# Kernel optimization log

Hardware: AMD Instinct MI355X
Metric: run time of the kernel (lower is better)

## Reference

```python
import jax, jax.numpy as jnp
import numpy as np

EPS = 1e-6
SIGMA = 0.5          # observation_noise_std
E, B, M, C = 64, 512, 128, 128  # episode, batch, memory_size, code_size


def setup_inputs() -> dict:
    key = jax.random.key(0)
    k1, k2 = jax.random.split(key)
    return {
        "input_encoded": jax.random.normal(k1, (E, B, C), dtype=jnp.float32),
        "memory_mean": jax.random.normal(k2, (M, C), dtype=jnp.float32),
        "memory_logvar": jnp.zeros((1,), dtype=jnp.float32),
    }


def reference(input_encoded, memory_mean, memory_logvar):
    # GPM.write_to_memory with direct_writing=False (sequential Kalman write).
    bsz = input_encoded.shape[1]
    prior_var = jnp.exp(memory_logvar) * jnp.ones((M,), input_encoded.dtype) + EPS  # (M,)
    prior_mean = jnp.broadcast_to(memory_mean, (bsz, M, C))                # (B,M,C)
    prior_cov = jnp.broadcast_to(jnp.diag(prior_var), (bsz, M, M))         # (B,M,M)
    eye_m = jnp.eye(M, dtype=input_encoded.dtype)

    def step(carry, z_i):            # z_i: (B,C)
        mean, cov = carry            # (B,M,C), (B,M,M)
        # _solve_w_mean (pseudoinverse=False): w = inv(M M^T + s^2 I) M z
        gram = jnp.einsum('bmc,bnc->bmn', mean, mean) + (SIGMA ** 2) * eye_m
        mz = jnp.einsum('bmc,bc->bm', mean, z_i)
        w = jnp.linalg.solve(gram, mz[..., None])[..., 0]  # (B,M)
        # _update_memory: rank-1 Kalman update
        delta = z_i - jnp.einsum('bm,bmc->bc', w, mean)    # (B,C)
        wU = jnp.einsum('bm,bmn->bn', w, cov)              # (B,M)
        sig = jnp.sum(wU * w, axis=-1) + SIGMA ** 2        # (B,)
        c = wU / sig[:, None]                              # (B,M)
        new_mean = mean + c[:, :, None] * delta[:, None, :]
        new_cov = cov - c[:, :, None] * wU[:, None, :]
        return (new_mean, new_cov), None

    (post_mean, post_cov), _ = jax.lax.scan(step, (prior_mean, prior_cov), input_encoded)

    # _dkl_M
    p_diag = jnp.diagonal(prior_cov, axis1=-2, axis2=-1)   # (B,M)
    q_diag = jnp.diagonal(post_cov, axis1=-2, axis2=-1)    # (B,M)
    t1 = C * jnp.sum(q_diag / p_diag, axis=-1)
    t2 = jnp.sum((post_mean - prior_mean) ** 2 / p_diag[..., None], axis=(-2, -1))
    t3 = -C * M
    t4 = C * jnp.sum(jnp.log(p_diag) - jnp.log(q_diag), axis=-1)
    dkl_M = jnp.mean(t1 + t2 + t3 + t4)
    return post_mean, post_cov, dkl_M
```

## Files before the change

### kernel.cpp

```cpp
#include <hip/hip_runtime.h>
#include <math.h>

#define MM   128
#define CC   128
#define EE   64
#define BB   512
#define LDT  132
#define SIG2 0.25f
#define SIG4 0.0625f
#define EPSV 1e-6f

#define AT_OFF   0
#define U_OFF    (128*LDT)
#define VEC_BASE (2*128*LDT)
#define VEC(i)   (VEC_BASE + (i)*128)
#define SC_OFF   (VEC_BASE + 9*128)
#define SMEM_FLOATS (SC_OFF + 32)
#define SMEM_BYTES  (SMEM_FLOATS * 4)

#define KATTR __attribute__((amdgpu_flat_work_group_size(512, 512), amdgpu_waves_per_eu(1, 2)))

__device__ __forceinline__ void ginv_inplace(float* sm, const int t) {
    float* T   = sm + AT_OFF;
    float* piv = sm + SC_OFF + 30;
    const int rg = t >> 2, cq = t & 3, ccb = cq << 5;
    float Gacc[32];
    #pragma unroll
    for (int j = 0; j < 32; ++j) Gacc[j] = 0.f;
    #pragma unroll 1
    for (int cc = 0; cc < 32; ++cc) {
        const float4 ar = *(const float4*)&T[rg*LDT + 4*cc];
        #pragma unroll
        for (int j = 0; j < 32; ++j) {
            const float4 br = *(const float4*)&T[(ccb + j)*LDT + 4*cc];
            Gacc[j] += ar.x*br.x + ar.y*br.y + ar.z*br.z + ar.w*br.w;
        }
    }
    #pragma unroll
    for (int j = 0; j < 32; ++j)
        if (ccb + j == rg) Gacc[j] += SIG2;
    __syncthreads();
    #pragma unroll
    for (int j4 = 0; j4 < 8; ++j4) {
        float4 v; v.x = Gacc[4*j4]; v.y = Gacc[4*j4+1]; v.z = Gacc[4*j4+2]; v.w = Gacc[4*j4+3];
        *(float4*)&T[rg*LDT + ccb + 4*j4] = v;
    }
    #pragma unroll 1
    for (int k = 0; k < 128; ++k) {
        const int kq = k >> 5;
        __syncthreads();
        if (rg == k && cq == kq) piv[0] = 1.0f / T[k*LDT + k];
        __syncthreads();
        if (rg == k) {
            const float pinv = piv[0];
            #pragma unroll
            for (int j4 = 0; j4 < 8; ++j4) {
                float4 g = *(float4*)&T[k*LDT + ccb + 4*j4];
                g.x *= pinv; g.y *= pinv; g.z *= pinv; g.w *= pinv;
                *(float4*)&T[k*LDT + ccb + 4*j4] = g;
            }
            if (cq == kq) T[k*LDT + k] = pinv;
        }
        __syncthreads();
        const float f = (rg == k) ? 0.f : T[rg*LDT + k];
        __syncthreads();
        if (rg != k) {
            #pragma unroll
            for (int j4 = 0; j4 < 8; ++j4) {
                float4 own = *(float4*)&T[rg*LDT + ccb + 4*j4];
                const float4 pv = *(const float4*)&T[k*LDT + ccb + 4*j4];
                own.x -= f*pv.x; own.y -= f*pv.y; own.z -= f*pv.z; own.w -= f*pv.w;
                *(float4*)&T[rg*LDT + ccb + 4*j4] = own;
            }
            if (cq == kq) T[rg*LDT + k] -= f;
        }
    }
    __syncthreads();
}

__global__ KATTR void gpm_setup(const float* __restrict__ mean0,
                                float* __restrict__ ginv0) {
    extern __shared__ float sm[];
    float* T = sm + AT_OFF;
    const int t = threadIdx.x;
    const int rg = t >> 2, cq = t & 3, ccb = cq << 5;
    const float* src = mean0 + rg*CC + ccb;
    #pragma unroll
    for (int j4 = 0; j4 < 8; ++j4)
        *(float4*)&T[rg*LDT + ccb + 4*j4] = *(const float4*)&src[4*j4];
    __syncthreads();
    ginv_inplace(sm, t);
    #pragma unroll
    for (int j4 = 0; j4 < 8; ++j4)
        *(float4*)&ginv0[rg*CC + ccb + 4*j4] = *(const float4*)&T[rg*LDT + ccb + 4*j4];
}

#define SC_ADD(base, slot, val) { float v_ = (val);                           \
    v_ += __shfl_xor(v_, 1, 64); v_ += __shfl_xor(v_, 2, 64);                 \
    v_ += __shfl_xor(v_, 4, 64);                                              \
    if ((l & 7) == 0) atomicAdd(&(base)[slot], v_); }

__global__ KATTR void gpm_main(
        const float* __restrict__ zin, const float* __restrict__ mean0,
        const float* __restrict__ lvar, float* __restrict__ out,
        const float* __restrict__ ginv0, const int use_ws) {
    extern __shared__ float sm[];
    float* At  = sm + AT_OFF;
    float* U   = sm + U_OFF;
    float* vz  = sm + VEC(0);
    float* vaz = sm + VEC(1);
    float* vw0 = sm + VEC(2);
    float* vt2 = sm + VEC(3);
    float* vuw = sm + VEC(4);
    float* scal = sm + SC_OFF;

    const int t = threadIdx.x, b = blockIdx.x;
    const int w = t >> 6, l = t & 63;
    const int r  = ((w & 1) << 6) | l;
    const int q  = w >> 1;
    const int cb = q << 5;

    sm[VEC(1) + t] = 0.f;
    sm[VEC(1) + 512 + t] = 0.f;
    if (t < 32) scal[t] = 0.f;
    if (t == 0) { scal[0] = SIG2; scal[8] = SIG2; }

    const float pvar = expf(lvar[0]) + EPSV;

    float Areg[32], Greg[32];

    if (use_ws) {
        const float* src = ginv0 + r*CC + cb;
        #pragma unroll
        for (int j4 = 0; j4 < 8; ++j4) {
            const float4 v = *(const float4*)&src[4*j4];
            Greg[4*j4] = v.x; Greg[4*j4+1] = v.y; Greg[4*j4+2] = v.z; Greg[4*j4+3] = v.w;
        }
    } else {
        const float* src = mean0 + r*CC + cb;
        #pragma unroll
        for (int j4 = 0; j4 < 8; ++j4)
            *(float4*)&At[r*LDT + cb + 4*j4] = *(const float4*)&src[4*j4];
        __syncthreads();
        ginv_inplace(sm, t);
        #pragma unroll
        for (int j4 = 0; j4 < 8; ++j4) {
            const float4 v = *(const float4*)&At[r*LDT + cb + 4*j4];
            Greg[4*j4] = v.x; Greg[4*j4+1] = v.y; Greg[4*j4+2] = v.z; Greg[4*j4+3] = v.w;
        }
        __syncthreads();
    }
    {
        const float* src = mean0 + r*CC + cb;
        #pragma unroll
        for (int j4 = 0; j4 < 8; ++j4) {
            const float4 v = *(const float4*)&src[4*j4];
            Areg[4*j4] = v.x; Areg[4*j4+1] = v.y; Areg[4*j4+2] = v.z; Areg[4*j4+3] = v.w;
        }
    }
    {
        const float4 z4 = {0.f, 0.f, 0.f, 0.f};
        #pragma unroll
        for (int j4 = 0; j4 < 8; ++j4)
            *(float4*)&U[r*LDT + cb + 4*j4] = z4;
        if (r >= cb && r < cb + 32) U[r*LDT + r] = pvar;
    }
    #pragma unroll
    for (int j = 0; j < 32; ++j) At[(cb + j)*LDT + r] = Areg[j];
    if (t < 32)
        *(float4*)&vz[4*t] = *(const float4*)&zin[(size_t)b*CC + 4*t];
    __syncthreads();

    {
        float s = 0.f;
        #pragma unroll
        for (int j4 = 0; j4 < 8; ++j4) {
            const float4 x = *(const float4*)&vz[cb + 4*j4];
            s += Areg[4*j4]*x.x + Areg[4*j4+1]*x.y + Areg[4*j4+2]*x.z + Areg[4*j4+3]*x.w;
        }
        atomicAdd(&vaz[r], s);
    }
    __syncthreads();

    #pragma unroll 1
    for (int e = 0; e < EE; ++e) {
        const int p  = e & 1;
        const int pp = p ^ 1;
        float* g1p = sm + VEC(5) + (p  << 7);
        float* g1q = sm + VEC(5) + (pp << 7);
        float* g2p = sm + VEC(7) + (p  << 7);
        float* g2q = sm + VEC(7) + (pp << 7);
        float* scp = scal + 8*p;
        float* scq = scal + 8*pp;
        {
            const float sigp    = scq[0];
            const float inv_sig = 1.0f / sigp;
            const float d2v     = scq[1];
            const float s_uwg2  = scq[2];
            const float s_vg1   = SIG4 * scq[3];
            const float s_uwg1  = SIG2 * scq[4];
            const float b11  = s_vg1 - d2v;
            const float b12  = 1.0f + s_uwg1*inv_sig;
            const float b22  = s_uwg2*inv_sig*inv_sig;
            const float idet = 1.0f / (b11*b22 - b12*b12);
            const float K11 = b22*idet, K12v = -b12*idet, K22 = b11*idet;
            const float k12s = K12v*inv_sig, k22s = K22*inv_sig*inv_sig;
            const float g1r = SIG2 * g1q[r];
            const float g2r = g2q[r];
            const float ar_ = K11*g1r + k12s*g2r;
            const float br_ = k12s*g1r + k22s*g2r;
            const float ars = ar_ * SIG2;
            float s = 0.f;
            #pragma unroll
            for (int j4 = 0; j4 < 8; ++j4) {
                const float4 q1 = *(const float4*)&g1q[cb + 4*j4];
                const float4 q2 = *(const float4*)&g2q[cb + 4*j4];
                Greg[4*j4]   -= ars*q1.x + br_*q2.x;
                Greg[4*j4+1] -= ars*q1.y + br_*q2.y;
                Greg[4*j4+2] -= ars*q1.z + br_*q2.z;
                Greg[4*j4+3] -= ars*q1.w + br_*q2.w;
                const float4 x = *(const float4*)&vaz[cb + 4*j4];
                s += Greg[4*j4]*x.x + Greg[4*j4+1]*x.y + Greg[4*j4+2]*x.z + Greg[4*j4+3]*x.w;
            }
            atomicAdd(&vw0[r], s);
            if (t < 128) { vt2[t] = vz[t]; vuw[t] = 0.f; }
        }
        __syncthreads();
        {
            float s1 = 0.f, s2 = 0.f, s3 = 0.f;
            #pragma unroll
            for (int j4 = 0; j4 < 8; ++j4) {
                const float4 a = *(const float4*)&At[r*LDT + cb + 4*j4];
                const float4 u = *(const float4*)&U[r*LDT + cb + 4*j4];
                const float4 x = *(const float4*)&vw0[cb + 4*j4];
                s1 += a.x*x.x + a.y*x.y + a.z*x.z + a.w*x.w;
                s2 += u.x*x.x + u.y*x.y + u.z*x.z + u.w*x.w;
                s3 += Greg[4*j4]*x.x + Greg[4*j4+1]*x.y + Greg[4*j4+2]*x.z + Greg[4*j4+3]*x.w;
            }
            atomicAdd(&vt2[r], -s1);
            atomicAdd(&vuw[r], s2);
            atomicAdd(&g1p[r], s3);
            const float w_r = vw0[r];
            SC_ADD(scp, 0, s2 * w_r);
            SC_ADD(scp, 3, s3 * w_r);
            if (t < 128) { g1q[t] = 0.f; g2q[t] = 0.f; vaz[t] = 0.f; }
            if (t == 448) { scq[0] = SIG2; scq[1] = 0.f; scq[2] = 0.f; scq[3] = 0.f; scq[4] = 0.f; }
            if (t < 32 && e + 1 < EE)
                *(float4*)&vz[4*t] = *(const float4*)&zin[((size_t)(e+1)*BB + b)*CC + 4*t];
        }
        __syncthreads();
        {
            float s = 0.f;
            #pragma unroll
            for (int j4 = 0; j4 < 8; ++j4) {
                const float4 x = *(const float4*)&vuw[cb + 4*j4];
                s += Greg[4*j4]*x.x + Greg[4*j4+1]*x.y + Greg[4*j4+2]*x.z + Greg[4*j4+3]*x.w;
            }
            atomicAdd(&g2p[r], s);
            SC_ADD(scp, 2, s * vuw[r]);
            if (t < 128) {
                float d_ = vt2[t]; d_ *= d_;
                d_ += __shfl_xor(d_, 1, 64); d_ += __shfl_xor(d_, 2, 64); d_ += __shfl_xor(d_, 4, 64);
                if ((l & 7) == 0) atomicAdd(&scp[1], d_);
                float p_ = g1p[t] * vuw[t];
                p_ += __shfl_xor(p_, 1, 64); p_ += __shfl_xor(p_, 2, 64); p_ += __shfl_xor(p_, 4, 64);
                if ((l & 7) == 0) atomicAdd(&scp[4], p_);
                vw0[t] = 0.f;
            }
            const float sig = scp[0];
            const float inv_sig = 1.0f / sig;
            const float cr = vuw[r] * inv_sig;
            #pragma unroll
            for (int j4 = 0; j4 < 8; ++j4) {
                const float4 dd = *(const float4*)&vt2[cb + 4*j4];
                Areg[4*j4]   += cr*dd.x; Areg[4*j4+1] += cr*dd.y;
                Areg[4*j4+2] += cr*dd.z; Areg[4*j4+3] += cr*dd.w;
                const float4 uu = *(const float4*)&vuw[cb + 4*j4];
                float4 u = *(float4*)&U[r*LDT + cb + 4*j4];
                u.x -= cr*uu.x; u.y -= cr*uu.y; u.z -= cr*uu.z; u.w -= cr*uu.w;
                *(float4*)&U[r*LDT + cb + 4*j4] = u;
            }
            #pragma unroll
            for (int j = 0; j < 32; ++j) At[(cb + j)*LDT + r] = Areg[j];
            if (e + 1 < EE) {
                float s2 = 0.f;
                #pragma unroll
                for (int j4 = 0; j4 < 8; ++j4) {
                    const float4 x = *(const float4*)&vz[cb + 4*j4];
                    s2 += Areg[4*j4]*x.x + Areg[4*j4+1]*x.y + Areg[4*j4+2]*x.z + Areg[4*j4+3]*x.w;
                }
                atomicAdd(&vaz[r], s2);
            }
        }
        __syncthreads();
    }

    {
        float* dst = out + (size_t)b*(MM*CC) + r*CC + cb;
        #pragma unroll
        for (int j4 = 0; j4 < 8; ++j4) {
            float4 v; v.x = Areg[4*j4]; v.y = Areg[4*j4+1]; v.z = Areg[4*j4+2]; v.w = Areg[4*j4+3];
            *(float4*)&dst[4*j4] = v;
        }
    }
    {
        float* dst = out + (size_t)BB*(MM*CC) + (size_t)b*(MM*MM) + r*MM + cb;
        #pragma unroll
        for (int j4 = 0; j4 < 8; ++j4)
            *(float4*)&dst[4*j4] = *(const float4*)&U[r*LDT + cb + 4*j4];
    }
    {
        const float inv_p = 1.0f / pvar;
        float acc = 0.f;
        const float* src = mean0 + r*CC + cb;
        #pragma unroll
        for (int j4 = 0; j4 < 8; ++j4) {
            const float4 a0 = *(const float4*)&src[4*j4];
            const float dx = Areg[4*j4]   - a0.x, dy = Areg[4*j4+1] - a0.y;
            const float dz = Areg[4*j4+2] - a0.z, dw = Areg[4*j4+3] - a0.w;
            acc += dx*dx + dy*dy + dz*dz + dw*dw;
        }
        float local = acc * inv_p;
        if (q == (r >> 5)) {
            const float qd = U[r*LDT + r];
            local += (float)CC * (qd*inv_p + logf(pvar) - logf(qd));
        }
        #pragma unroll
        for (int m2 = 1; m2 < 64; m2 <<= 1) local += __shfl_xor(local, m2, 64);
        if (l == 0) scal[16 + w] = local;
        __syncthreads();
        if (t == 0) {
            float tot = 0.f;
            #pragma unroll
            for (int i = 0; i < 8; ++i) tot += scal[16 + i];
            tot -= (float)(CC*MM);
            atomicAdd(out + (size_t)2*BB*MM*CC, tot * (1.0f/(float)BB));
        }
    }
}

extern "C" void kernel_launch(void* const* d_in, const int* in_sizes, int n_in,
                              void* d_out, int out_size, void* d_ws, size_t ws_size,
                              hipStream_t stream) {
    (void)in_sizes; (void)n_in; (void)out_size;
    const float* zin   = (const float*)d_in[0];
    const float* mean0 = (const float*)d_in[1];
    const float* lvar  = (const float*)d_in[2];
    float* out = (float*)d_out;
    float* dkl = out + (size_t)2*BB*MM*CC;
    const int use_ws = (d_ws != nullptr && ws_size >= (size_t)MM*MM*4) ? 1 : 0;
    float* ginv0 = (float*)d_ws;

    hipFuncSetAttribute((const void*)gpm_setup, hipFuncAttributeMaxDynamicSharedMemorySize, SMEM_BYTES);
    hipFuncSetAttribute((const void*)gpm_main,  hipFuncAttributeMaxDynamicSharedMemorySize, SMEM_BYTES);

    hipMemsetAsync(dkl, 0, sizeof(float), stream);
    if (use_ws)
        gpm_setup<<<1, 512, SMEM_BYTES, stream>>>(mean0, ginv0);
    gpm_main<<<BB, 512, SMEM_BYTES, stream>>>(zin, mean0, lvar, out, ginv0, use_ws);
}
```

Measured before the change: 1.367 ms.

## Halve block size and keep covariance in registers instead of LDS

Threads per block drop from 512 to 256, so each thread now owns 64 columns of mean, covariance and inverse Gram instead of 32. The covariance matrix U moves from shared memory into registers (Ureg), which removes one 128x132 LDS tile and its per-step loads and stores. The diagonal for the KL term is now picked out of registers. The cost is much higher register pressure (about 192 live floats per thread, with waves_per_eu pinned at 1) and fewer threads to hide latency, so spilling or lower throughput is possible.

```diff
diff --git a/kernel.cpp b/kernel.cpp
--- a/kernel.cpp
+++ b/kernel.cpp
@@ -11,50 +11,49 @@
 #define EPSV 1e-6f
 
 #define AT_OFF   0
-#define U_OFF    (128*LDT)
-#define VEC_BASE (2*128*LDT)
+#define VEC_BASE (128*LDT)
 #define VEC(i)   (VEC_BASE + (i)*128)
 #define SC_OFF   (VEC_BASE + 9*128)
 #define SMEM_FLOATS (SC_OFF + 32)
 #define SMEM_BYTES  (SMEM_FLOATS * 4)
 
-#define KATTR __attribute__((amdgpu_flat_work_group_size(512, 512), amdgpu_waves_per_eu(1, 2)))
+#define KATTR __attribute__((amdgpu_flat_work_group_size(256, 256), amdgpu_waves_per_eu(1, 1)))
 
 __device__ __forceinline__ void ginv_inplace(float* sm, const int t) {
     float* T   = sm + AT_OFF;
     float* piv = sm + SC_OFF + 30;
-    const int rg = t >> 2, cq = t & 3, ccb = cq << 5;
-    float Gacc[32];
-    #pragma unroll
-    for (int j = 0; j < 32; ++j) Gacc[j] = 0.f;
+    const int rg = t >> 1, cq = t & 1, ccb = cq << 6;
+    float Gacc[64];
+    #pragma unroll
+    for (int j = 0; j < 64; ++j) Gacc[j] = 0.f;
     #pragma unroll 1
     for (int cc = 0; cc < 32; ++cc) {
         const float4 ar = *(const float4*)&T[rg*LDT + 4*cc];
         #pragma unroll
-        for (int j = 0; j < 32; ++j) {
+        for (int j = 0; j < 64; ++j) {
             const float4 br = *(const float4*)&T[(ccb + j)*LDT + 4*cc];
             Gacc[j] += ar.x*br.x + ar.y*br.y + ar.z*br.z + ar.w*br.w;
         }
     }
     #pragma unroll
-    for (int j = 0; j < 32; ++j)
+    for (int j = 0; j < 64; ++j)
         if (ccb + j == rg) Gacc[j] += SIG2;
     __syncthreads();
     #pragma unroll
-    for (int j4 = 0; j4 < 8; ++j4) {
+    for (int j4 = 0; j4 < 16; ++j4) {
         float4 v; v.x = Gacc[4*j4]; v.y = Gacc[4*j4+1]; v.z = Gacc[4*j4+2]; v.w = Gacc[4*j4+3];
         *(float4*)&T[rg*LDT + ccb + 4*j4] = v;
     }
     #pragma unroll 1
     for (int k = 0; k < 128; ++k) {
-        const int kq = k >> 5;
+        const int kq = k >> 6;
         __syncthreads();
         if (rg == k && cq == kq) piv[0] = 1.0f / T[k*LDT + k];
         __syncthreads();
         if (rg == k) {
             const float pinv = piv[0];
             #pragma unroll
-            for (int j4 = 0; j4 < 8; ++j4) {
+            for (int j4 = 0; j4 < 16; ++j4) {
                 float4 g = *(float4*)&T[k*LDT + ccb + 4*j4];
                 g.x *= pinv; g.y *= pinv; g.z *= pinv; g.w *= pinv;
                 *(float4*)&T[k*LDT + ccb + 4*j4] = g;
@@ -66,7 +65,7 @@
         __syncthreads();
         if (rg != k) {
             #pragma unroll
-            for (int j4 = 0; j4 < 8; ++j4) {
+            for (int j4 = 0; j4 < 16; ++j4) {
                 float4 own = *(float4*)&T[rg*LDT + ccb + 4*j4];
                 const float4 pv = *(const float4*)&T[k*LDT + ccb + 4*j4];
                 own.x -= f*pv.x; own.y -= f*pv.y; own.z -= f*pv.z; own.w -= f*pv.w;
@@ -83,15 +82,15 @@
     extern __shared__ float sm[];
     float* T = sm + AT_OFF;
     const int t = threadIdx.x;
-    const int rg = t >> 2, cq = t & 3, ccb = cq << 5;
+    const int rg = t >> 1, cq = t & 1, ccb = cq << 6;
     const float* src = mean0 + rg*CC + ccb;
     #pragma unroll
-    for (int j4 = 0; j4 < 8; ++j4)
+    for (int j4 = 0; j4 < 16; ++j4)
         *(float4*)&T[rg*LDT + ccb + 4*j4] = *(const float4*)&src[4*j4];
     __syncthreads();
     ginv_inplace(sm, t);
     #pragma unroll
-    for (int j4 = 0; j4 < 8; ++j4)
+    for (int j4 = 0; j4 < 16; ++j4)
         *(float4*)&ginv0[rg*CC + ccb + 4*j4] = *(const float4*)&T[rg*LDT + ccb + 4*j4];
 }
 
@@ -106,7 +105,6 @@
         const float* __restrict__ ginv0, const int use_ws) {
     extern __shared__ float sm[];
     float* At  = sm + AT_OFF;
-    float* U   = sm + U_OFF;
     float* vz  = sm + VEC(0);
     float* vaz = sm + VEC(1);
     float* vw0 = sm + VEC(2);
@@ -118,33 +116,36 @@
     const int w = t >> 6, l = t & 63;
     const int r  = ((w & 1) << 6) | l;
     const int q  = w >> 1;
-    const int cb = q << 5;
+    const int cb = q << 6;
 
     sm[VEC(1) + t] = 0.f;
+    sm[VEC(1) + 256 + t] = 0.f;
     sm[VEC(1) + 512 + t] = 0.f;
+    sm[VEC(1) + 768 + t] = 0.f;
     if (t < 32) scal[t] = 0.f;
+    __syncthreads();
     if (t == 0) { scal[0] = SIG2; scal[8] = SIG2; }
 
     const float pvar = expf(lvar[0]) + EPSV;
 
-    float Areg[32], Greg[32];
+    float Areg[64], Ureg[64], Greg[64];
 
     if (use_ws) {
         const float* src = ginv0 + r*CC + cb;
         #pragma unroll
-        for (int j4 = 0; j4 < 8; ++j4) {
+        for (int j4 = 0; j4 < 16; ++j4) {
             const float4 v = *(const float4*)&src[4*j4];
             Greg[4*j4] = v.x; Greg[4*j4+1] = v.y; Greg[4*j4+2] = v.z; Greg[4*j4+3] = v.w;
         }
     } else {
         const float* src = mean0 + r*CC + cb;
         #pragma unroll
-        for (int j4 = 0; j4 < 8; ++j4)
+        for (int j4 = 0; j4 < 16; ++j4)
             *(float4*)&At[r*LDT + cb + 4*j4] = *(const float4*)&src[4*j4];
         __syncthreads();
         ginv_inplace(sm, t);
         #pragma unroll
-        for (int j4 = 0; j4 < 8; ++j4) {
+        for (int j4 = 0; j4 < 16; ++j4) {
             const float4 v = *(const float4*)&At[r*LDT + cb + 4*j4];
             Greg[4*j4] = v.x; Greg[4*j4+1] = v.y; Greg[4*j4+2] = v.z; Greg[4*j4+3] = v.w;
         }
@@ -153,20 +154,15 @@
     {
         const float* src = mean0 + r*CC + cb;
         #pragma unroll
-        for (int j4 = 0; j4 < 8; ++j4) {
+        for (int j4 = 0; j4 < 16; ++j4) {
             const float4 v = *(const float4*)&src[4*j4];
             Areg[4*j4] = v.x; Areg[4*j4+1] = v.y; Areg[4*j4+2] = v.z; Areg[4*j4+3] = v.w;
         }
     }
-    {
-        const float4 z4 = {0.f, 0.f, 0.f, 0.f};
-        #pragma unroll
-        for (int j4 = 0; j4 < 8; ++j4)
-            *(float4*)&U[r*LDT + cb + 4*j4] = z4;
-        if (r >= cb && r < cb + 32) U[r*LDT + r] = pvar;
-    }
-    #pragma unroll
-    for (int j = 0; j < 32; ++j) At[(cb + j)*LDT + r] = Areg[j];
+    #pragma unroll
+    for (int j = 0; j < 64; ++j) Ureg[j] = (cb + j == r) ? pvar : 0.f;
+    #pragma unroll
+    for (int j = 0; j < 64; ++j) At[(cb + j)*LDT + r] = Areg[j];
     if (t < 32)
         *(float4*)&vz[4*t] = *(const float4*)&zin[(size_t)b*CC + 4*t];
     __syncthreads();
@@ -174,7 +170,7 @@
     {
         float s = 0.f;
         #pragma unroll
-        for (int j4 = 0; j4 < 8; ++j4) {
+        for (int j4 = 0; j4 < 16; ++j4) {
             const float4 x = *(const float4*)&vz[cb + 4*j4];
             s += Areg[4*j4]*x.x + Areg[4*j4+1]*x.y + Areg[4*j4+2]*x.z + Areg[4*j4+3]*x.w;
         }
@@ -212,7 +208,7 @@
             const float ars = ar_ * SIG2;
             float s = 0.f;
             #pragma unroll
-            for (int j4 = 0; j4 < 8; ++j4) {
+            for (int j4 = 0; j4 < 16; ++j4) {
                 const float4 q1 = *(const float4*)&g1q[cb + 4*j4];
                 const float4 q2 = *(const float4*)&g2q[cb + 4*j4];
                 Greg[4*j4]   -= ars*q1.x + br_*q2.x;
@@ -229,12 +225,11 @@
         {
             float s1 = 0.f, s2 = 0.f, s3 = 0.f;
             #pragma unroll
-            for (int j4 = 0; j4 < 8; ++j4) {
+            for (int j4 = 0; j4 < 16; ++j4) {
                 const float4 a = *(const float4*)&At[r*LDT + cb + 4*j4];
-                const float4 u = *(const float4*)&U[r*LDT + cb + 4*j4];
                 const float4 x = *(const float4*)&vw0[cb + 4*j4];
                 s1 += a.x*x.x + a.y*x.y + a.z*x.z + a.w*x.w;
-                s2 += u.x*x.x + u.y*x.y + u.z*x.z + u.w*x.w;
+                s2 += Ureg[4*j4]*x.x + Ureg[4*j4+1]*x.y + Ureg[4*j4+2]*x.z + Ureg[4*j4+3]*x.w;
                 s3 += Greg[4*j4]*x.x + Greg[4*j4+1]*x.y + Greg[4*j4+2]*x.z + Greg[4*j4+3]*x.w;
             }
             atomicAdd(&vt2[r], -s1);
@@ -244,7 +239,7 @@
             SC_ADD(scp, 0, s2 * w_r);
             SC_ADD(scp, 3, s3 * w_r);
             if (t < 128) { g1q[t] = 0.f; g2q[t] = 0.f; vaz[t] = 0.f; }
-            if (t == 448) { scq[0] = SIG2; scq[1] = 0.f; scq[2] = 0.f; scq[3] = 0.f; scq[4] = 0.f; }
+            if (t == 192) { scq[0] = SIG2; scq[1] = 0.f; scq[2] = 0.f; scq[3] = 0.f; scq[4] = 0.f; }
             if (t < 32 && e + 1 < EE)
                 *(float4*)&vz[4*t] = *(const float4*)&zin[((size_t)(e+1)*BB + b)*CC + 4*t];
         }
@@ -252,7 +247,7 @@
         {
             float s = 0.f;
             #pragma unroll
-            for (int j4 = 0; j4 < 8; ++j4) {
+            for (int j4 = 0; j4 < 16; ++j4) {
                 const float4 x = *(const float4*)&vuw[cb + 4*j4];
                 s += Greg[4*j4]*x.x + Greg[4*j4+1]*x.y + Greg[4*j4+2]*x.z + Greg[4*j4+3]*x.w;
             }
@@ -271,21 +266,20 @@
             const float inv_sig = 1.0f / sig;
             const float cr = vuw[r] * inv_sig;
             #pragma unroll
-            for (int j4 = 0; j4 < 8; ++j4) {
+            for (int j4 = 0; j4 < 16; ++j4) {
                 const float4 dd = *(const float4*)&vt2[cb + 4*j4];
                 Areg[4*j4]   += cr*dd.x; Areg[4*j4+1] += cr*dd.y;
                 Areg[4*j4+2] += cr*dd.z; Areg[4*j4+3] += cr*dd.w;
                 const float4 uu = *(const float4*)&vuw[cb + 4*j4];
-                float4 u = *(float4*)&U[r*LDT + cb + 4*j4];
-                u.x -= cr*uu.x; u.y -= cr*uu.y; u.z -= cr*uu.z; u.w -= cr*uu.w;
-                *(float4*)&U[r*LDT + cb + 4*j4] = u;
-            }
-            #pragma unroll
-            for (int j = 0; j < 32; ++j) At[(cb + j)*LDT + r] = Areg[j];
+                Ureg[4*j4]   -= cr*uu.x; Ureg[4*j4+1] -= cr*uu.y;
+                Ureg[4*j4+2] -= cr*uu.z; Ureg[4*j4+3] -= cr*uu.w;
+            }
+            #pragma unroll
+            for (int j = 0; j < 64; ++j) At[(cb + j)*LDT + r] = Areg[j];
             if (e + 1 < EE) {
                 float s2 = 0.f;
                 #pragma unroll
-                for (int j4 = 0; j4 < 8; ++j4) {
+                for (int j4 = 0; j4 < 16; ++j4) {
                     const float4 x = *(const float4*)&vz[cb + 4*j4];
                     s2 += Areg[4*j4]*x.x + Areg[4*j4+1]*x.y + Areg[4*j4+2]*x.z + Areg[4*j4+3]*x.w;
                 }
@@ -298,42 +292,44 @@
     {
         float* dst = out + (size_t)b*(MM*CC) + r*CC + cb;
         #pragma unroll
-        for (int j4 = 0; j4 < 8; ++j4) {
+        for (int j4 = 0; j4 < 16; ++j4) {
             float4 v; v.x = Areg[4*j4]; v.y = Areg[4*j4+1]; v.z = Areg[4*j4+2]; v.w = Areg[4*j4+3];
             *(float4*)&dst[4*j4] = v;
         }
     }
+    float qd = 1.f;
     {
         float* dst = out + (size_t)BB*(MM*CC) + (size_t)b*(MM*MM) + r*MM + cb;
         #pragma unroll
-        for (int j4 = 0; j4 < 8; ++j4)
-            *(float4*)&dst[4*j4] = *(const float4*)&U[r*LDT + cb + 4*j4];
+        for (int j4 = 0; j4 < 16; ++j4) {
+            float4 v; v.x = Ureg[4*j4]; v.y = Ureg[4*j4+1]; v.z = Ureg[4*j4+2]; v.w = Ureg[4*j4+3];
+            *(float4*)&dst[4*j4] = v;
+            if (cb + 4*j4     == r) qd = v.x;
+            if (cb + 4*j4 + 1 == r) qd = v.y;
+            if (cb + 4*j4 + 2 == r) qd = v.z;
+            if (cb + 4*j4 + 3 == r) qd = v.w;
+        }
     }
     {
         const float inv_p = 1.0f / pvar;
         float acc = 0.f;
         const float* src = mean0 + r*CC + cb;
         #pragma unroll
-        for (int j4 = 0; j4 < 8; ++j4) {
+        for (int j4 = 0; j4 < 16; ++j4) {
             const float4 a0 = *(const float4*)&src[4*j4];
             const float dx = Areg[4*j4]   - a0.x, dy = Areg[4*j4+1] - a0.y;
             const float dz = Areg[4*j4+2] - a0.z, dw = Areg[4*j4+3] - a0.w;
             acc += dx*dx + dy*dy + dz*dz + dw*dw;
         }
         float local = acc * inv_p;
-        if (q == (r >> 5)) {
-            const float qd = U[r*LDT + r];
+        if (q == (r >> 6))
             local += (float)CC * (qd*inv_p + logf(pvar) - logf(qd));
-        }
         #pragma unroll
         for (int m2 = 1; m2 < 64; m2 <<= 1) local += __shfl_xor(local, m2, 64);
         if (l == 0) scal[16 + w] = local;
         __syncthreads();
         if (t == 0) {
-            float tot = 0.f;
-            #pragma unroll
-            for (int i = 0; i < 8; ++i) tot += scal[16 + i];
-            tot -= (float)(CC*MM);
+            const float tot = scal[16] + scal[17] + scal[18] + scal[19] - (float)(CC*MM);
             atomicAdd(out + (size_t)2*BB*MM*CC, tot * (1.0f/(float)BB));
         }
     }
@@ -356,6 +352,6 @@
 
     hipMemsetAsync(dkl, 0, sizeof(float), stream);
     if (use_ws)
-        gpm_setup<<<1, 512, SMEM_BYTES, stream>>>(mean0, ginv0);
-    gpm_main<<<BB, 512, SMEM_BYTES, stream>>>(zin, mean0, lvar, out, ginv0, use_ws);
+        gpm_setup<<<1, 256, SMEM_BYTES, stream>>>(mean0, ginv0);
+    gpm_main<<<BB, 256, SMEM_BYTES, stream>>>(zin, mean0, lvar, out, ginv0, use_ws);
 }
```

New measurement: 1.427 ms. +4.4%, slower.
